# Optimization experiments

Measured on AMD Instinct MI355X. Metric: run time of the kernel, lower is better.

## Reference

```python
import jax, jax.numpy as jnp
import numpy as np
import math

D_MODEL = 1024
N_HEADS = 16
HEAD_DIM = D_MODEL // N_HEADS
THETA = 10000.0


def _rope(x, cos, sin):
    # x: [b, h, s, head_dim]; cos/sin: [s, head_dim//2]
    xe = x[..., 0::2]
    xo = x[..., 1::2]
    re = xe * cos - xo * sin
    ro = xe * sin + xo * cos
    # interleave back to even/odd layout
    return jnp.stack([re, ro], axis=-1).reshape(x.shape)


def setup_inputs() -> dict:
    key = jax.random.key(0)
    k1, k2, k3, k4, k5 = jax.random.split(key, 5)
    std = math.sqrt(2.0 / (D_MODEL + D_MODEL))
    x = jax.random.normal(k1, (2, 2048, D_MODEL), dtype=jnp.float32)
    Wq = jax.random.normal(k2, (D_MODEL, D_MODEL), dtype=jnp.float32) * std
    Wk = jax.random.normal(k3, (D_MODEL, D_MODEL), dtype=jnp.float32) * std
    Wv = jax.random.normal(k4, (D_MODEL, D_MODEL), dtype=jnp.float32) * std
    Wo = jax.random.normal(k5, (D_MODEL, D_MODEL), dtype=jnp.float32) * (std / math.sqrt(2))
    return {"x": x, "Wq": Wq, "Wk": Wk, "Wv": Wv, "Wo": Wo}


def reference(x, Wq, Wk, Wv, Wo):
    b, s, d = x.shape
    h, hd = N_HEADS, HEAD_DIM
    # projections: einsum 'batch seq d_in, d_model d_in -> batch seq d_model' == x @ W.T
    def proj(W):
        y = jnp.einsum('bsd,md->bsm', x, W)
        return y.reshape(b, s, h, hd).transpose(0, 2, 1, 3)  # [b, h, s, hd]
    Q, K, V = proj(Wq), proj(Wk), proj(Wv)
    # RoPE with default positions = arange(seq)
    freqs = 1.0 / (THETA ** (jnp.arange(0, hd, 2, dtype=jnp.float32) / hd))
    angles = jnp.arange(s, dtype=jnp.float32)[:, None] * freqs[None, :]  # [s, hd//2]
    cos, sin = jnp.cos(angles), jnp.sin(angles)
    Q = _rope(Q, cos, sin)
    K = _rope(K, cos, sin)
    # naive causal attention
    scores = jnp.einsum('bhqd,bhkd->bhqk', Q, K) / math.sqrt(hd)
    causal = jnp.tril(jnp.ones((s, s), dtype=bool))
    scores = jnp.where(causal, scores, -jnp.inf)
    attn = jax.nn.softmax(scores, axis=-1)
    out = jnp.einsum('bhqk,bhkd->bhqd', attn, V)
    out = out.transpose(0, 2, 1, 3).reshape(b, s, d)
    return jnp.einsum('bsd,md->bsm', out, Wo)
```

## Files before the change

kernel.cpp:

```cpp
#include <hip/hip_runtime.h>
#include <stdint.h>
#include <stddef.h>

typedef __bf16 bf16;
typedef __bf16 bf16x8 __attribute__((ext_vector_type(8)));
typedef __bf16 bf16x4 __attribute__((ext_vector_type(4)));
typedef short short4v __attribute__((ext_vector_type(4)));
typedef float f32x4 __attribute__((ext_vector_type(4)));

#define GAS __attribute__((address_space(1)))
#define LAS __attribute__((address_space(3)))

__device__ __forceinline__ void async_load16(const void* g, void* l) {
  __builtin_amdgcn_global_load_lds((const GAS void*)g, (LAS void*)l, 16, 0, 0);
}

__device__ __forceinline__ f32x4 mfma16(bf16x4 a, bf16x4 b, f32x4 c) {
#if defined(__HIP_DEVICE_COMPILE__)
#if __has_builtin(__builtin_amdgcn_mfma_f32_16x16x16bf16_1k)
  return __builtin_amdgcn_mfma_f32_16x16x16bf16_1k(
      __builtin_bit_cast(short4v, a), __builtin_bit_cast(short4v, b), c, 0, 0, 0);
#else
  f32x4 d;
  asm volatile("v_mfma_f32_16x16x16_bf16 %0, %1, %2, %3"
               : "=v"(d)
               : "v"(a), "v"(b), "v"(c));
  return d;
#endif
#else
  (void)a; (void)b;
  return c;
#endif
}

__global__ __launch_bounds__(256) void cast_all(
    const float* __restrict__ x, const float* __restrict__ Wq,
    const float* __restrict__ Wk, const float* __restrict__ Wv,
    const float* __restrict__ Wo, bf16* __restrict__ Xh,
    bf16* __restrict__ Wqkv, bf16* __restrict__ Woh) {
  int idx = (blockIdx.x * 256 + threadIdx.x) * 4;
  const float* src;
  bf16* dst;
  float scale = 1.0f;
  if (idx < 4194304) {
    src = x + idx; dst = Xh + idx;
  } else if (idx < 7340032) {
    int j = idx - 4194304;
    if (j < 1048576) {
      src = Wq + j; scale = 0.18033688011112042f;
    } else {
      src = ((j < 2097152) ? Wk : Wv) + (j & 1048575);
    }
    dst = Wqkv + j;
  } else {
    int j = idx - 7340032;
    src = Wo + j; dst = Woh + j;
  }
  float4 v = *(const float4*)src;
  bf16x4 o;
  o[0] = (bf16)(v.x * scale); o[1] = (bf16)(v.y * scale);
  o[2] = (bf16)(v.z * scale); o[3] = (bf16)(v.w * scale);
  *(bf16x4*)dst = o;
}

__global__ __launch_bounds__(256) void gemm_qkv(
    const bf16* __restrict__ A, const bf16* __restrict__ B,
    bf16* __restrict__ Qh, bf16* __restrict__ Kh, bf16* __restrict__ Vt,
    int K) {
  __shared__ __align__(16) bf16 As[128 * 32];
  __shared__ __align__(16) bf16 Bs[128 * 32];
  const int tid = threadIdx.x;
  const int wave = tid >> 6, lane = tid & 63;
  const int bm = blockIdx.y * 128, bn = blockIdx.x * 128;
  const int wm = (wave >> 1) * 64, wn = (wave & 1) * 64;
  const int lrow = lane >> 2, lk = (lane & 3) * 8;
  const int fr = lane & 15, fk = (lane >> 4) * 8;

  f32x4 acc[4][4] = {};

  for (int kt = 0; kt < K; kt += 32) {
    __syncthreads();
#pragma unroll
    for (int c = 0; c < 2; ++c) {
      const int chunk = wave * 2 + c;
      const bf16* ga = A + (size_t)(bm + chunk * 16 + lrow) * K + kt + lk;
      async_load16(ga, (void*)(As + chunk * 512));
      const bf16* gb = B + (size_t)(bn + chunk * 16 + lrow) * K + kt + lk;
      async_load16(gb, (void*)(Bs + chunk * 512));
    }
    __syncthreads();

    bf16x8 af[4], bfr[4];
#pragma unroll
    for (int i = 0; i < 4; ++i)
      af[i] = *(const bf16x8*)&As[(wm + i * 16 + fr) * 32 + fk];
#pragma unroll
    for (int j = 0; j < 4; ++j)
      bfr[j] = *(const bf16x8*)&Bs[(wn + j * 16 + fr) * 32 + fk];
#pragma unroll
    for (int i = 0; i < 4; ++i)
#pragma unroll
      for (int j = 0; j < 4; ++j)
        acc[i][j] =
            __builtin_amdgcn_mfma_f32_16x16x32_bf16(af[i], bfr[j], acc[i][j], 0, 0, 0);
  }

  const int r0 = (lane >> 4) * 4, cc = lane & 15;
  const bool oddl = cc & 1;
#pragma unroll
  for (int i = 0; i < 4; ++i) {
    const int row0 = bm + wm + i * 16 + r0;
    const int b = row0 >> 11, s0 = row0 & 2047;
#pragma unroll
    for (int j = 0; j < 4; ++j) {
      const int col = bn + wn + j * 16 + cc;
      if (col < 2048) {
        const int hcol = col & 1023;
        const int h = hcol >> 6, d = hcol & 63;
        const int ip = d >> 1;
        const float freq = __expf((float)ip * -0.2878231366242557f);
        const bool isK = col >= 1024;
        bf16* dst = (isK ? Kh : Qh) + ((size_t)(b * 16 + h) * 2048) * 64;
#pragma unroll
        for (int r = 0; r < 4; ++r) {
          float own = acc[i][j][r];
          float oth = __shfl_xor(own, 1, 64);
          float sn, cs;
          __sincosf((float)(s0 + r) * freq, &sn, &cs);
          float res = oddl ? (oth * sn + own * cs) : (own * cs - oth * sn);
          const int dd = isK ? (d ^ (((s0 + r) & 7) << 3)) : d;
          dst[(size_t)(s0 + r) * 64 + dd] = (bf16)res;
        }
      } else {
        const int v = col - 2048, h = v >> 6, d = v & 63;
        bf16x4 o;
#pragma unroll
        for (int r = 0; r < 4; ++r) o[r] = (bf16)acc[i][j][r];
        const int s2 = (s0 & ~63) | ((s0 ^ ((d & 7) << 3)) & 63);
        *(bf16x4*)&Vt[(((size_t)b * 16 + h) * 64 + d) * 2048 + s2] = o;
      }
    }
  }
}

template <typename OutT, int BM, int BN>
__global__ __launch_bounds__(256) void gemm_bt(
    const bf16* __restrict__ A, const bf16* __restrict__ B,
    OutT* __restrict__ C, int M, int N, int K) {
  constexpr int ACH = BM / 16, NCH = (BM + BN) / 16, PW = NCH / 4;
  constexpr int FM = BM / 32, FN = BN / 32;
  __shared__ __align__(16) bf16 As[BM * 32];
  __shared__ __align__(16) bf16 Bs[BN * 32];
  const int tid = threadIdx.x;
  const int wave = tid >> 6, lane = tid & 63;
  const int bm = blockIdx.y * BM, bn = blockIdx.x * BN;
  const int wm = (wave >> 1) * (BM / 2), wn = (wave & 1) * (BN / 2);
  const int lrow = lane >> 2, lk = (lane & 3) * 8;
  const int fr = lane & 15, fk = (lane >> 4) * 8;

  f32x4 acc[FM][FN] = {};

  for (int kt = 0; kt < K; kt += 32) {
    __syncthreads();
#pragma unroll
    for (int c = 0; c < PW; ++c) {
      const int chunk = wave * PW + c;
      if (chunk < ACH) {
        const bf16* ga = A + (size_t)(bm + chunk * 16 + lrow) * K + kt + lk;
        async_load16(ga, (void*)(As + chunk * 512));
      } else {
        const int bc = chunk - ACH;
        const bf16* gb = B + (size_t)(bn + bc * 16 + lrow) * K + kt + lk;
        async_load16(gb, (void*)(Bs + bc * 512));
      }
    }
    __syncthreads();

    bf16x8 af[FM], bfr[FN];
#pragma unroll
    for (int i = 0; i < FM; ++i)
      af[i] = *(const bf16x8*)&As[(wm + i * 16 + fr) * 32 + fk];
#pragma unroll
    for (int j = 0; j < FN; ++j)
      bfr[j] = *(const bf16x8*)&Bs[(wn + j * 16 + fr) * 32 + fk];
#pragma unroll
    for (int i = 0; i < FM; ++i)
#pragma unroll
      for (int j = 0; j < FN; ++j)
        acc[i][j] =
            __builtin_amdgcn_mfma_f32_16x16x32_bf16(af[i], bfr[j], acc[i][j], 0, 0, 0);
  }

  const int r0 = (lane >> 4) * 4, cc = lane & 15;
#pragma unroll
  for (int i = 0; i < FM; ++i)
#pragma unroll
    for (int j = 0; j < FN; ++j)
#pragma unroll
      for (int r = 0; r < 4; ++r)
        C[(size_t)(bm + wm + i * 16 + r0 + r) * N + (bn + wn + j * 16 + cc)] =
            (OutT)acc[i][j][r];
}

__global__ __launch_bounds__(256, 2) void attn(const bf16* __restrict__ Qh,
                                               const bf16* __restrict__ Kh,
                                               const bf16* __restrict__ Vt,
                                               bf16* __restrict__ Oh) {
  __shared__ __align__(16) bf16 Ks[3][64 * 64];
  __shared__ __align__(16) bf16 Vs[3][64 * 64];
  const int f = blockIdx.x;
  int j, bh;
  if (f < 256) { bh = f >> 4;              j = 15 - (f & 15); }
  else         { bh = 16 + ((f - 256) >> 4); j = f & 15; }
  const int tid = threadIdx.x, w = tid >> 6, lane = tid & 63;
  const int nlo = lane & 15, g = lane >> 4;
  const int q0 = j * 128, qw0 = q0 + w * 32;
  const bf16* __restrict__ Qp = Qh + (size_t)bh * 131072;
  const bf16* __restrict__ Kp = Kh + (size_t)bh * 131072;
  const bf16* __restrict__ Vp = Vt + (size_t)bh * 131072;
  const int n = 2 * (j + 1);
  const int nw = 2 * j + (w >> 1) + 1;

  bf16x8 aq[2][2];
#pragma unroll
  for (int qb = 0; qb < 2; ++qb)
#pragma unroll
    for (int ks = 0; ks < 2; ++ks)
      aq[qb][ks] =
          *(const bf16x8*)&Qp[(size_t)(qw0 + qb * 16 + nlo) * 64 + ks * 32 + g * 8];

  f32x4 oacc[2][4] = {};
  float lsum[2] = {0.f, 0.f};
  const int sw = (nlo & 7) << 3;

  const int srow = w * 16 + (lane >> 3);
  const int soff = (lane & 7) * 8;

  auto stage = [&](int slot, int kbase) {
    async_load16(Kp + (size_t)(kbase + srow) * 64 + soff,
                 (void*)(Ks[slot] + w * 1024));
    async_load16(Kp + (size_t)(kbase + srow + 8) * 64 + soff,
                 (void*)(Ks[slot] + w * 1024 + 512));
    async_load16(Vp + (size_t)srow * 2048 + kbase + soff,
                 (void*)(Vs[slot] + w * 1024));
    async_load16(Vp + (size_t)(srow + 8) * 2048 + kbase + soff,
                 (void*)(Vs[slot] + w * 1024 + 512));
  };

  bf16x8 pk[4][2];
  auto rdK = [&](int slot) {
    const bf16* __restrict__ Kw = Ks[slot];
#pragma unroll
    for (int ni = 0; ni < 4; ++ni)
#pragma unroll
      for (int ks = 0; ks < 2; ++ks)
        pk[ni][ks] =
            *(const bf16x8*)&Kw[(ni * 16 + nlo) * 64 + ((ks * 32 + g * 8) ^ sw)];
  };

  bf16x4 av[4][4];
  auto rdV = [&](int slot) {
    const bf16* __restrict__ Vw = Vs[slot];
#pragma unroll
    for (int ni = 0; ni < 4; ++ni)
#pragma unroll
      for (int mi = 0; mi < 4; ++mi)
        av[ni][mi] =
            *(const bf16x4*)&Vw[(mi * 16 + nlo) * 64 + ((ni * 16 + g * 4) ^ sw)];
  };

  f32x4 st[2][4];
  auto qk = [&]() {
#pragma unroll
    for (int qb = 0; qb < 2; ++qb) {
#pragma unroll
      for (int ni = 0; ni < 4; ++ni) st[qb][ni] = f32x4{0.f, 0.f, 0.f, 0.f};
#pragma unroll
      for (int ks = 0; ks < 2; ++ks)
#pragma unroll
        for (int ni = 0; ni < 4; ++ni)
          st[qb][ni] = __builtin_amdgcn_mfma_f32_16x16x32_bf16(
              pk[ni][ks], aq[qb][ks], st[qb][ni], 0, 0, 0);
    }
  };

  bf16x4 p[2][4];
  auto expv = [&](int i) {
    const int kbase = i * 64;
    const bool dg = (i == nw - 1);
#pragma unroll
    for (int qb = 0; qb < 2; ++qb) {
      const int qg = qw0 + qb * 16 + nlo;
      if (!dg) {
#pragma unroll
        for (int ni = 0; ni < 4; ++ni)
#pragma unroll
          for (int r = 0; r < 4; ++r) {
            float e = __builtin_amdgcn_exp2f(st[qb][ni][r]);
            lsum[qb] += e;
            p[qb][ni][r] = (bf16)e;
          }
      } else {
#pragma unroll
        for (int ni = 0; ni < 4; ++ni) {
          const int kg0 = kbase + ni * 16 + g * 4;
#pragma unroll
          for (int r = 0; r < 4; ++r) {
            float e = __builtin_amdgcn_exp2f(st[qb][ni][r]);
            e = (kg0 + r <= qg) ? e : 0.0f;
            lsum[qb] += e;
            p[qb][ni][r] = (bf16)e;
          }
        }
      }
    }
  };

  auto pv = [&]() {
#pragma unroll
    for (int ni = 0; ni < 4; ++ni)
#pragma unroll
      for (int mi = 0; mi < 4; ++mi)
#pragma unroll
        for (int qb = 0; qb < 2; ++qb)
          oacc[qb][mi] = mfma16(av[ni][mi], p[qb][ni], oacc[qb][mi]);
  };

  stage(0, 0);
  stage(1, 64);
  __syncthreads();
  rdK(0);
  qk();
  expv(0);

  for (int i = 0; i < n - 1; ++i) {
    const int i1 = i + 1;
    if (i + 2 < n) stage((i + 2) % 3, (i + 2) * 64);
    const bool doQK = (i1 < nw);
    if (doQK) rdK(i1 % 3);
    rdV(i % 3);
    __builtin_amdgcn_s_setprio(1);
    if (doQK) qk();
    pv();
    __builtin_amdgcn_s_setprio(0);
    if (doQK) expv(i1);
    __syncthreads();
  }

  if (nw == n) {
    rdV((n - 1) % 3);
    pv();
  }

#pragma unroll
  for (int qb = 0; qb < 2; ++qb) {
    lsum[qb] += __shfl_xor(lsum[qb], 16, 64);
    lsum[qb] += __shfl_xor(lsum[qb], 32, 64);
  }

  const int bb = bh >> 4, hd = bh & 15;
#pragma unroll
  for (int qb = 0; qb < 2; ++qb) {
    const float inv = 1.0f / lsum[qb];
    const int q = qw0 + qb * 16 + nlo;
#pragma unroll
    for (int mi = 0; mi < 4; ++mi) {
      bf16x4 o;
#pragma unroll
      for (int r = 0; r < 4; ++r) o[r] = (bf16)(oacc[qb][mi][r] * inv);
      *(bf16x4*)&Oh[((size_t)bb * 2048 + q) * 1024 + hd * 64 + mi * 16 + g * 4] = o;
    }
  }
}

extern "C" void kernel_launch(void* const* d_in, const int* in_sizes, int n_in,
                              void* d_out, int out_size, void* d_ws, size_t ws_size,
                              hipStream_t stream) {
  (void)in_sizes; (void)n_in; (void)out_size; (void)ws_size;
  const float* x = (const float*)d_in[0];
  const float* Wq = (const float*)d_in[1];
  const float* Wk = (const float*)d_in[2];
  const float* Wv = (const float*)d_in[3];
  const float* Wo = (const float*)d_in[4];
  float* out = (float*)d_out;
  char* ws = (char*)d_ws;

  bf16* Xh   = (bf16*)(ws);
  bf16* Wqkv = (bf16*)(ws + 8388608);
  bf16* Woh  = (bf16*)(ws + 14680064);
  bf16* Qh   = (bf16*)(ws + 16777216);
  bf16* Kh   = (bf16*)(ws + 25165824);
  bf16* Vt   = (bf16*)(ws + 33554432);
  bf16* Oh   = (bf16*)(ws + 41943040);

  cast_all<<<8192, 256, 0, stream>>>(x, Wq, Wk, Wv, Wo, Xh, Wqkv, Woh);
  gemm_qkv<<<dim3(24, 32), 256, 0, stream>>>(Xh, Wqkv, Qh, Kh, Vt, 1024);
  attn<<<512, 256, 0, stream>>>(Qh, Kh, Vt, Oh);
  gemm_bt<float, 128, 128><<<dim3(8, 32), 256, 0, stream>>>(Oh, Woh, out, 4096, 1024, 1024);
}
```

Baseline: 190.0 us.

## Deepen QKV GEMM K-tile to 64 with swizzled LDS and precomputed RoPE table

The QKV projection GEMM now stages 64-wide K tiles with an XOR-swizzled LDS layout, which halves the number of barrier-separated iterations and is meant to avoid LDS bank conflicts. It also sets a launch-bounds occupancy hint. The RoPE cos/sin values are now computed once per (position, frequency) by extra blocks in the cast kernel and stored in a table, so the GEMM epilogue reads them instead of recomputing exp and sincos per element. In exchange, LDS use per block doubles and the epilogue adds global loads from the table.

```diff
diff --git a/kernel.cpp b/kernel.cpp
--- a/kernel.cpp
+++ b/kernel.cpp
@@ -37,7 +37,20 @@
     const float* __restrict__ x, const float* __restrict__ Wq,
     const float* __restrict__ Wk, const float* __restrict__ Wv,
     const float* __restrict__ Wo, bf16* __restrict__ Xh,
-    bf16* __restrict__ Wqkv, bf16* __restrict__ Woh) {
+    bf16* __restrict__ Wqkv, bf16* __restrict__ Woh,
+    float2* __restrict__ rope) {
+  if (blockIdx.x >= 8192) {
+    const int e = ((blockIdx.x - 8192) * 256 + threadIdx.x) * 4;
+    const int s = e >> 5, ip0 = e & 31;
+#pragma unroll
+    for (int r = 0; r < 4; ++r) {
+      const float freq = __expf((float)(ip0 + r) * -0.2878231366242557f);
+      float sn, cs;
+      __sincosf((float)s * freq, &sn, &cs);
+      rope[e + r] = make_float2(cs, sn);
+    }
+    return;
+  }
   int idx = (blockIdx.x * 256 + threadIdx.x) * 4;
   const float* src;
   bf16* dst;
@@ -63,46 +76,54 @@
   *(bf16x4*)dst = o;
 }
 
-__global__ __launch_bounds__(256) void gemm_qkv(
+__global__ __launch_bounds__(256, 3) void gemm_qkv(
     const bf16* __restrict__ A, const bf16* __restrict__ B,
-    bf16* __restrict__ Qh, bf16* __restrict__ Kh, bf16* __restrict__ Vt,
-    int K) {
-  __shared__ __align__(16) bf16 As[128 * 32];
-  __shared__ __align__(16) bf16 Bs[128 * 32];
+    const float2* __restrict__ rope, bf16* __restrict__ Qh,
+    bf16* __restrict__ Kh, bf16* __restrict__ Vt, int K) {
+  __shared__ __align__(16) bf16 As[128 * 64];
+  __shared__ __align__(16) bf16 Bs[128 * 64];
   const int tid = threadIdx.x;
   const int wave = tid >> 6, lane = tid & 63;
   const int bm = blockIdx.y * 128, bn = blockIdx.x * 128;
   const int wm = (wave >> 1) * 64, wn = (wave & 1) * 64;
-  const int lrow = lane >> 2, lk = (lane & 3) * 8;
-  const int fr = lane & 15, fk = (lane >> 4) * 8;
+  const int fr = lane & 15, g = lane >> 4;
+  const int sw8 = (fr & 7) * 8;
+
+  const int srow = tid >> 3;
+  const int scol = 8 * ((tid & 7) ^ (srow & 7));
+  const int ldst = wave * 512;
 
   f32x4 acc[4][4] = {};
 
-  for (int kt = 0; kt < K; kt += 32) {
+  for (int kt = 0; kt < K; kt += 64) {
     __syncthreads();
 #pragma unroll
-    for (int c = 0; c < 2; ++c) {
-      const int chunk = wave * 2 + c;
-      const bf16* ga = A + (size_t)(bm + chunk * 16 + lrow) * K + kt + lk;
-      async_load16(ga, (void*)(As + chunk * 512));
-      const bf16* gb = B + (size_t)(bn + chunk * 16 + lrow) * K + kt + lk;
-      async_load16(gb, (void*)(Bs + chunk * 512));
+    for (int s = 0; s < 4; ++s) {
+      const int row = s * 32 + srow;
+      async_load16(A + (size_t)(bm + row) * K + kt + scol,
+                   (void*)(As + s * 2048 + ldst));
+      async_load16(B + (size_t)(bn + row) * K + kt + scol,
+                   (void*)(Bs + s * 2048 + ldst));
     }
     __syncthreads();
 
-    bf16x8 af[4], bfr[4];
-#pragma unroll
-    for (int i = 0; i < 4; ++i)
-      af[i] = *(const bf16x8*)&As[(wm + i * 16 + fr) * 32 + fk];
-#pragma unroll
-    for (int j = 0; j < 4; ++j)
-      bfr[j] = *(const bf16x8*)&Bs[(wn + j * 16 + fr) * 32 + fk];
-#pragma unroll
-    for (int i = 0; i < 4; ++i)
+#pragma unroll
+    for (int ks = 0; ks < 2; ++ks) {
+      bf16x8 af[4], bfr[4];
+      const int kq = (ks * 32 + g * 8) ^ sw8;
+#pragma unroll
+      for (int i = 0; i < 4; ++i)
+        af[i] = *(const bf16x8*)&As[(wm + i * 16 + fr) * 64 + kq];
 #pragma unroll
       for (int j = 0; j < 4; ++j)
-        acc[i][j] =
-            __builtin_amdgcn_mfma_f32_16x16x32_bf16(af[i], bfr[j], acc[i][j], 0, 0, 0);
+        bfr[j] = *(const bf16x8*)&Bs[(wn + j * 16 + fr) * 64 + kq];
+#pragma unroll
+      for (int i = 0; i < 4; ++i)
+#pragma unroll
+        for (int j = 0; j < 4; ++j)
+          acc[i][j] = __builtin_amdgcn_mfma_f32_16x16x32_bf16(af[i], bfr[j],
+                                                              acc[i][j], 0, 0, 0);
+    }
   }
 
   const int r0 = (lane >> 4) * 4, cc = lane & 15;
@@ -118,16 +139,14 @@
         const int hcol = col & 1023;
         const int h = hcol >> 6, d = hcol & 63;
         const int ip = d >> 1;
-        const float freq = __expf((float)ip * -0.2878231366242557f);
         const bool isK = col >= 1024;
         bf16* dst = (isK ? Kh : Qh) + ((size_t)(b * 16 + h) * 2048) * 64;
 #pragma unroll
         for (int r = 0; r < 4; ++r) {
           float own = acc[i][j][r];
           float oth = __shfl_xor(own, 1, 64);
-          float sn, cs;
-          __sincosf((float)(s0 + r) * freq, &sn, &cs);
-          float res = oddl ? (oth * sn + own * cs) : (own * cs - oth * sn);
+          const float2 t = rope[((s0 + r) << 5) + ip];
+          float res = oddl ? (oth * t.y + own * t.x) : (own * t.x - oth * t.y);
           const int dd = isK ? (d ^ (((s0 + r) & 7) << 3)) : d;
           dst[(size_t)(s0 + r) * 64 + dd] = (bf16)res;
         }
@@ -385,16 +404,17 @@
   float* out = (float*)d_out;
   char* ws = (char*)d_ws;
 
-  bf16* Xh   = (bf16*)(ws);
-  bf16* Wqkv = (bf16*)(ws + 8388608);
-  bf16* Woh  = (bf16*)(ws + 14680064);
-  bf16* Qh   = (bf16*)(ws + 16777216);
-  bf16* Kh   = (bf16*)(ws + 25165824);
-  bf16* Vt   = (bf16*)(ws + 33554432);
-  bf16* Oh   = (bf16*)(ws + 41943040);
-
-  cast_all<<<8192, 256, 0, stream>>>(x, Wq, Wk, Wv, Wo, Xh, Wqkv, Woh);
-  gemm_qkv<<<dim3(24, 32), 256, 0, stream>>>(Xh, Wqkv, Qh, Kh, Vt, 1024);
+  bf16* Xh    = (bf16*)(ws);
+  bf16* Wqkv  = (bf16*)(ws + 8388608);
+  bf16* Woh   = (bf16*)(ws + 14680064);
+  bf16* Qh    = (bf16*)(ws + 16777216);
+  bf16* Kh    = (bf16*)(ws + 25165824);
+  bf16* Vt    = (bf16*)(ws + 33554432);
+  bf16* Oh    = (bf16*)(ws + 41943040);
+  float2* rope = (float2*)(ws + 50331648);
+
+  cast_all<<<8256, 256, 0, stream>>>(x, Wq, Wk, Wv, Wo, Xh, Wqkv, Woh, rope);
+  gemm_qkv<<<dim3(24, 32), 256, 0, stream>>>(Xh, Wqkv, rope, Qh, Kh, Vt, 1024);
   attn<<<512, 256, 0, stream>>>(Qh, Kh, Vt, Oh);
   gemm_bt<float, 128, 128><<<dim3(8, 32), 256, 0, stream>>>(Oh, Woh, out, 4096, 1024, 1024);
 }
```

Measured after the change: 178.1 us. 1.07x faster.
